# Optimization experiments

Measured on AMD Instinct MI355X. Metric: run time of the kernel, lower is better.

Reference implementation:

```python
import jax, jax.numpy as jnp
import numpy as np

D_IN, D_HID, N_TOK = 2048, 8192, 8192

def _ternary(key, shape):
    # ternary {-1, 0, 1} weights stored as float32
    return jax.random.randint(key, shape, -1, 2).astype(jnp.float32)

def setup_inputs() -> dict:
    key = jax.random.key(0)
    kx, k1, k2, kh, k3 = jax.random.split(key, 5)
    return {
        "x": jax.random.normal(kx, (N_TOK, D_IN), dtype=jnp.float32),
        "W1": _ternary(k1, (D_HID, D_IN)),   # gate proj
        "W2": _ternary(k2, (D_HID, D_IN)),   # value proj
        "Wh": _ternary(kh, (D_HID, D_HID)),  # hidden layer (depth-1 == 1)
        "W3": _ternary(k3, (D_IN, D_HID)),   # output proj
        # per-layer dequant scales (scalar), ~1/sqrt(fan_in)
        "s1": jnp.float32(1.0 / np.sqrt(D_IN)),
        "s2": jnp.float32(1.0 / np.sqrt(D_IN)),
        "sh": jnp.float32(1.0 / np.sqrt(D_HID)),
        "s3": jnp.float32(1.0 / np.sqrt(D_HID)),
    }

def _tlin(x, W, s):
    # ternary packed linear: dequantized matmul, no bias
    return jnp.einsum('td,hd->th', x, W) * s

def reference(x, W1, W2, Wh, W3, s1, s2, sh, s3):
    h = jax.nn.silu(_tlin(x, W1, s1)) * _tlin(x, W2, s2)   # SwiGLU entry
    h = jax.nn.gelu(_tlin(h, Wh, sh), approximate=False)    # hidden block (depth-1)
    return _tlin(h, W3, s3)                                 # [N_TOK, D_IN]
```

## Files before the change

### kernel.cpp

```cpp
#include <hip/hip_runtime.h>
#include <hip/hip_bf16.h>
#include <stdint.h>

typedef __bf16 bf16;
typedef __bf16 bf16x8 __attribute__((ext_vector_type(8)));
typedef float f32x4 __attribute__((ext_vector_type(4)));

typedef uint32_t __attribute__((address_space(1))) * gptr_as1;
typedef uint32_t __attribute__((address_space(3))) * lptr_as3;

__device__ __forceinline__ void async16(const void* g, void* l) {
    __builtin_amdgcn_global_load_lds((gptr_as1)(uintptr_t)g,
                                     (lptr_as3)(uintptr_t)l,
                                     16, 0, 0);
}

__device__ __forceinline__ void bar() {
    asm volatile("" ::: "memory");
    __builtin_amdgcn_s_barrier();
    asm volatile("" ::: "memory");
}

__global__ void cvt_f32_bf16_kernel(const float* __restrict__ src,
                                    bf16* __restrict__ dst, int n8) {
    int i = blockIdx.x * blockDim.x + threadIdx.x;
    if (i >= n8) return;
    const float4* s = reinterpret_cast<const float4*>(src);
    float4 a = s[2 * (size_t)i], b = s[2 * (size_t)i + 1];
    bf16x8 v;
    v[0] = (bf16)a.x; v[1] = (bf16)a.y; v[2] = (bf16)a.z; v[3] = (bf16)a.w;
    v[4] = (bf16)b.x; v[5] = (bf16)b.y; v[6] = (bf16)b.z; v[7] = (bf16)b.w;
    *reinterpret_cast<bf16x8*>(dst + (size_t)i * 8) = v;
}

__global__ void cvt_ilv_kernel(const float* __restrict__ src,
                               bf16* __restrict__ dst, int n8, int sel) {
    int i = blockIdx.x * blockDim.x + threadIdx.x;
    if (i >= n8) return;
    const int row = i >> 8;
    const int c = i & 255;
    const int drow = ((row >> 4) << 5) + (sel << 4) + (row & 15);
    const float4* s = reinterpret_cast<const float4*>(src);
    float4 a = s[2 * (size_t)i], b = s[2 * (size_t)i + 1];
    bf16x8 v;
    v[0] = (bf16)a.x; v[1] = (bf16)a.y; v[2] = (bf16)a.z; v[3] = (bf16)a.w;
    v[4] = (bf16)b.x; v[5] = (bf16)b.y; v[6] = (bf16)b.z; v[7] = (bf16)b.w;
    *reinterpret_cast<bf16x8*>(dst + ((size_t)drow * 256 + c) * 8) = v;
}

template <int EPI, int K>
__global__ __launch_bounds__(512, 1)
void gemm8p(const bf16* __restrict__ A, const bf16* __restrict__ B,
            void* __restrict__ Cout, const float* __restrict__ s1p,
            const float* __restrict__ s2p, int N, int ldh) {
    __shared__ __align__(16) char sm[131072];

    const int tid = threadIdx.x;
    const int w = tid >> 6, l = tid & 63;
    const int wr = w >> 2, wc = w & 3;

    const int gx = gridDim.x;
    const int nwg = gx * (int)gridDim.y;
    const int orig = blockIdx.y * gx + blockIdx.x;
    const int wg = (orig & 7) * (nwg >> 3) + (orig >> 3);
    const int bm = wg / gx, bn = wg % gx;

    constexpr int NT = K / 64;

    f32x4 acc[8][4] = {};

    char* const bufA0 = sm;
    char* const bufB0 = sm + 32768;
    char* const bufA1 = sm + 65536;
    char* const bufB1 = sm + 98304;
    const int arow = bm * 256, brow = bn * 256;

    const int srow_in = l >> 3;
    const int scolb = ((l & 7) ^ srow_in) << 4;
    auto STAGE = [&](char* ldsT, const bf16* g, int grow0, int kt, int r0) {
        const int rr = r0 + w * 8 + srow_in;
        const char* gp = (const char*)(g + (size_t)(grow0 + rr) * K + kt * 64) + scolb;
        async16(gp, ldsT + r0 * 128 + w * 1024);
    };

    const int rlane = l & 15;
    const int chi = (l >> 4) << 4;
    const int sw = (rlane & 7) << 4;
    const int ksd = (rlane & 4) ? -64 : 64;
    const int offA = (wr * 128 + rlane) * 128 + (chi ^ sw);
    const int offB = (wc * 64 + rlane) * 128 + (chi ^ sw);
    const char* const pA0  = bufA0 + offA;  const char* const pA0k = pA0 + ksd;
    const char* const pB0  = bufB0 + offB;  const char* const pB0k = pB0 + ksd;
    const char* const pA1  = bufA1 + offA;  const char* const pA1k = pA1 + ksd;
    const char* const pB1  = bufB1 + offB;  const char* const pB1k = pB1 + ksd;

    STAGE(bufA0, A, arow, 0, 0);   STAGE(bufA0, A, arow, 0, 128);
    STAGE(bufB0, B, brow, 0, 0);   STAGE(bufB0, B, brow, 0, 64);
    STAGE(bufB0, B, brow, 0, 128); STAGE(bufB0, B, brow, 0, 192);
    STAGE(bufA0, A, arow, 0, 64);  STAGE(bufA0, A, arow, 0, 192);
    STAGE(bufA1, A, arow, 1, 0);   STAGE(bufA1, A, arow, 1, 128);
    STAGE(bufB1, B, brow, 1, 0);   STAGE(bufB1, B, brow, 1, 64);
    STAGE(bufB1, B, brow, 1, 128); STAGE(bufB1, B, brow, 1, 192);
    asm volatile("s_waitcnt vmcnt(6)" ::: "memory");
    bar();

    auto body = [&](int kt, char* cA, char* cB, char* nA,
                    const char* pa, const char* pak,
                    const char* pb, const char* pbk) {
        bf16x8 ae[4], ao[4], bv[4];
#pragma unroll
        for (int i = 0; i < 4; ++i)
            ae[i] = *reinterpret_cast<const bf16x8*>(pa + i * 2048);
#pragma unroll
        for (int j = 0; j < 4; ++j)
            bv[j] = *reinterpret_cast<const bf16x8*>(pb + j * 2048);
        if (kt + 1 < NT) { STAGE(nA, A, arow, kt + 1, 64); STAGE(nA, A, arow, kt + 1, 192); }
        bar();
        asm volatile("s_waitcnt lgkmcnt(0)" ::: "memory");
        __builtin_amdgcn_sched_barrier(0);
        __builtin_amdgcn_s_setprio(1);
#pragma unroll
        for (int i = 0; i < 4; ++i)
#pragma unroll
            for (int j = 0; j < 4; ++j)
                acc[i][j] = __builtin_amdgcn_mfma_f32_16x16x32_bf16(ae[i], bv[j], acc[i][j], 0, 0, 0);
        __builtin_amdgcn_s_setprio(0);
        bar();
#pragma unroll
        for (int i = 0; i < 4; ++i)
            ao[i] = *reinterpret_cast<const bf16x8*>(pa + 8192 + i * 2048);
        bar();
        asm volatile("s_waitcnt lgkmcnt(0)" ::: "memory");
        __builtin_amdgcn_sched_barrier(0);
        __builtin_amdgcn_s_setprio(1);
#pragma unroll
        for (int i = 0; i < 4; ++i)
#pragma unroll
            for (int j = 0; j < 4; ++j)
                acc[4 + i][j] = __builtin_amdgcn_mfma_f32_16x16x32_bf16(ao[i], bv[j], acc[4 + i][j], 0, 0, 0);
        __builtin_amdgcn_s_setprio(0);
        bar();
#pragma unroll
        for (int i = 0; i < 4; ++i)
            ae[i] = *reinterpret_cast<const bf16x8*>(pak + i * 2048);
#pragma unroll
        for (int j = 0; j < 4; ++j)
            bv[j] = *reinterpret_cast<const bf16x8*>(pbk + j * 2048);
        if (kt + 2 < NT) { STAGE(cB, B, brow, kt + 2, 0); STAGE(cB, B, brow, kt + 2, 64); }
        bar();
        asm volatile("s_waitcnt lgkmcnt(0)" ::: "memory");
        __builtin_amdgcn_sched_barrier(0);
        __builtin_amdgcn_s_setprio(1);
#pragma unroll
        for (int i = 0; i < 4; ++i)
#pragma unroll
            for (int j = 0; j < 4; ++j)
                acc[i][j] = __builtin_amdgcn_mfma_f32_16x16x32_bf16(ae[i], bv[j], acc[i][j], 0, 0, 0);
        __builtin_amdgcn_s_setprio(0);
        bar();
#pragma unroll
        for (int i = 0; i < 4; ++i)
            ao[i] = *reinterpret_cast<const bf16x8*>(pak + 8192 + i * 2048);
        if (kt + 2 < NT) {
            STAGE(cB, B, brow, kt + 2, 128); STAGE(cB, B, brow, kt + 2, 192);
            STAGE(cA, A, arow, kt + 2, 0);   STAGE(cA, A, arow, kt + 2, 128);
        }
        bar();
        asm volatile("s_waitcnt lgkmcnt(0)" ::: "memory");
        __builtin_amdgcn_sched_barrier(0);
        __builtin_amdgcn_s_setprio(1);
#pragma unroll
        for (int i = 0; i < 4; ++i)
#pragma unroll
            for (int j = 0; j < 4; ++j)
                acc[4 + i][j] = __builtin_amdgcn_mfma_f32_16x16x32_bf16(ao[i], bv[j], acc[4 + i][j], 0, 0, 0);
        __builtin_amdgcn_s_setprio(0);
        if (kt == NT - 2) { asm volatile("s_waitcnt vmcnt(0)" ::: "memory"); }
        else              { asm volatile("s_waitcnt vmcnt(6)" ::: "memory"); }
        bar();
    };

#pragma unroll 1
    for (int kt = 0; kt < NT; kt += 2) {
        body(kt,     bufA0, bufB0, bufA1, pA0, pA0k, pB0, pB0k);
        body(kt + 1, bufA1, bufB1, bufA0, pA1, pA1k, pB1, pB1k);
    }

    const float s1 = s1p[0];
    const int r0 = bm * 256 + wr * 128 + ((l >> 4) << 2);
    if constexpr (EPI == 2) {
        const float s2 = s2p[0];
        const int hcb = (bn * 8 + wc * 2) * 16 + rlane;
#pragma unroll
        for (int i = 0; i < 8; ++i)
#pragma unroll
            for (int jp = 0; jp < 2; ++jp)
#pragma unroll
                for (int q = 0; q < 4; ++q) {
                    float g = acc[i][2 * jp][q] * s1;
                    float v = acc[i][2 * jp + 1][q] * s2;
                    float sig = 1.0f / (1.0f + __expf(-g));
                    ((bf16*)Cout)[(size_t)(r0 + i * 16 + q) * ldh + hcb + jp * 16] =
                        (bf16)(g * sig * v);
                }
    } else {
        const int c0 = bn * 256 + wc * 64 + rlane;
#pragma unroll
        for (int i = 0; i < 8; ++i)
#pragma unroll
            for (int j = 0; j < 4; ++j)
#pragma unroll
                for (int q = 0; q < 4; ++q) {
                    float v = acc[i][j][q] * s1;
                    size_t idx = (size_t)(r0 + i * 16 + q) * N + (c0 + j * 16);
                    if constexpr (EPI == 0) {
                        float g = 0.5f * v * (1.0f + erff(v * 0.70710678118654752f));
                        ((bf16*)Cout)[idx] = (bf16)g;
                    } else {
                        ((float*)Cout)[idx] = v;
                    }
                }
    }
}

extern "C" void kernel_launch(void* const* d_in, const int* in_sizes, int n_in,
                              void* d_out, int out_size, void* d_ws, size_t ws_size,
                              hipStream_t stream) {
    constexpr int NTOK = 8192, DIN = 2048, DHID = 8192;

    const float* x  = (const float*)d_in[0];
    const float* W1 = (const float*)d_in[1];
    const float* W2 = (const float*)d_in[2];
    const float* Wh = (const float*)d_in[3];
    const float* W3 = (const float*)d_in[4];
    const float* s1 = (const float*)d_in[5];
    const float* s2 = (const float*)d_in[6];
    const float* sh = (const float*)d_in[7];
    const float* s3 = (const float*)d_in[8];
    float* out = (float*)d_out;

    char* ws = (char*)d_ws;
    size_t off = 0;
    bf16* xb   = (bf16*)(ws + off); off += (size_t)NTOK * DIN * 2;
    bf16* w12b = (bf16*)(ws + off); off += (size_t)2 * DHID * DIN * 2;
    bf16* w3b  = (bf16*)(ws + off); off += (size_t)DIN * DHID * 2;
    bf16* whb  = (bf16*)(ws + off); off += (size_t)DHID * DHID * 2;
    bf16* h1   = (bf16*)(ws + off); off += (size_t)NTOK * DHID * 2;
    bf16* h2   = (bf16*)(ws + off); off += (size_t)NTOK * DHID * 2;
    if (ws_size < off) return;

    auto cvt = [&](const float* s, bf16* d, size_t n) {
        int n8 = (int)(n / 8);
        cvt_f32_bf16_kernel<<<(n8 + 255) / 256, 256, 0, stream>>>(s, d, n8);
    };
    cvt(x,  xb,  (size_t)NTOK * DIN);
    cvt(Wh, whb, (size_t)DHID * DHID);
    cvt(W3, w3b, (size_t)DIN * DHID);
    {
        int n8 = (int)((size_t)DHID * DIN / 8);
        cvt_ilv_kernel<<<(n8 + 255) / 256, 256, 0, stream>>>(W1, w12b, n8, 0);
        cvt_ilv_kernel<<<(n8 + 255) / 256, 256, 0, stream>>>(W2, w12b, n8, 1);
    }

    gemm8p<2, DIN><<<dim3(2 * DHID / 256, NTOK / 256), 512, 0, stream>>>(
        xb, w12b, h1, s1, s2, 2 * DHID, DHID);
    gemm8p<0, DHID><<<dim3(DHID / 256, NTOK / 256), 512, 0, stream>>>(
        h1, whb, h2, sh, sh, DHID, DHID);
    gemm8p<1, DHID><<<dim3(DIN / 256, NTOK / 256), 512, 0, stream>>>(
        h2, w3b, out, s3, s3, DIN, DIN);
}
```

Baseline: 1.713 ms.

## Use 256x128-tile two-waves-per-SIMD GEMM kernel for hidden layer

Adds a new GEMM kernel with 256-thread blocks, 256x128 output tiles, K-step 32, a double-buffered 48KB LDS and launch bounds allowing two blocks per CU. The hidden-layer GEMM now uses it instead of the 512-thread 256x256 kernel. The aim is to hide latency through occupancy across co-resident blocks rather than deep intra-block pipelining. The trade-off is less operand reuse per tile and more barriers per unit of K.

```diff
diff --git a/kernel.cpp b/kernel.cpp
--- a/kernel.cpp
+++ b/kernel.cpp
@@ -49,6 +49,127 @@
 }
 
 template <int EPI, int K>
+__global__ __launch_bounds__(256, 2)
+void gemm2t(const bf16* __restrict__ A, const bf16* __restrict__ B,
+            void* __restrict__ Cout, const float* __restrict__ s1p,
+            const float* __restrict__ s2p, int N, int ldh) {
+    __shared__ __align__(16) char sm[49152];
+
+    const int tid = threadIdx.x;
+    const int w = tid >> 6, l = tid & 63;
+    const int wr = w >> 1, wc = w & 1;
+
+    const int gx = gridDim.x;
+    const int nwg = gx * (int)gridDim.y;
+    const int orig = blockIdx.y * gx + blockIdx.x;
+    const int wg = (orig & 7) * (nwg >> 3) + (orig >> 3);
+    const int bm = wg / gx, bn = wg % gx;
+
+    constexpr int NT = K / 32;
+
+    f32x4 acc[8][4] = {};
+
+    const int arow = bm * 256, brow = bn * 128;
+
+    const int sr = l >> 2;
+    const int sg = ((l & 3) ^ ((l >> 3) & 3)) << 4;
+    const char* qa0 = (const char*)(A + (size_t)(arow +   0 + w * 16 + sr) * K) + sg;
+    const char* qa1 = (const char*)(A + (size_t)(arow +  64 + w * 16 + sr) * K) + sg;
+    const char* qa2 = (const char*)(A + (size_t)(arow + 128 + w * 16 + sr) * K) + sg;
+    const char* qa3 = (const char*)(A + (size_t)(arow + 192 + w * 16 + sr) * K) + sg;
+    const char* qb0 = (const char*)(B + (size_t)(brow +   0 + w * 16 + sr) * K) + sg;
+    const char* qb1 = (const char*)(B + (size_t)(brow +  64 + w * 16 + sr) * K) + sg;
+    const int ldw = w * 1024;
+
+    auto STAGE_TILE = [&](int p) {
+        char* ba = sm + p * 24576;
+        char* bb = ba + 16384;
+        async16(qa0, ba +     0 + ldw); async16(qa1, ba +  4096 + ldw);
+        async16(qa2, ba +  8192 + ldw); async16(qa3, ba + 12288 + ldw);
+        async16(qb0, bb +     0 + ldw); async16(qb1, bb +  4096 + ldw);
+    };
+    auto ADV = [&]() {
+        qa0 += 64; qa1 += 64; qa2 += 64; qa3 += 64; qb0 += 64; qb1 += 64;
+    };
+
+    const int rlane = l & 15;
+    const int chi = (l >> 4) << 4;
+
+    STAGE_TILE(0);
+    ADV();
+    asm volatile("s_waitcnt vmcnt(0)" ::: "memory");
+    bar();
+
+#pragma unroll 1
+    for (int kt = 0; kt < NT; ++kt) {
+        if (kt + 1 < NT) { STAGE_TILE((kt + 1) & 1); ADV(); }
+        const char* ba = sm + (kt & 1) * 24576;
+        const char* bb = ba + 16384;
+
+        bf16x8 av[8], bv[4];
+#pragma unroll
+        for (int i = 0; i < 8; ++i) {
+            const int row = wr * 128 + i * 16 + rlane;
+            av[i] = *reinterpret_cast<const bf16x8*>(
+                ba + row * 64 + (chi ^ (((row >> 1) & 3) << 4)));
+        }
+#pragma unroll
+        for (int j = 0; j < 4; ++j) {
+            const int row = wc * 64 + j * 16 + rlane;
+            bv[j] = *reinterpret_cast<const bf16x8*>(
+                bb + row * 64 + (chi ^ (((row >> 1) & 3) << 4)));
+        }
+        asm volatile("s_waitcnt lgkmcnt(0)" ::: "memory");
+        __builtin_amdgcn_sched_barrier(0);
+        __builtin_amdgcn_s_setprio(1);
+#pragma unroll
+        for (int i = 0; i < 8; ++i)
+#pragma unroll
+            for (int j = 0; j < 4; ++j)
+                acc[i][j] = __builtin_amdgcn_mfma_f32_16x16x32_bf16(av[i], bv[j], acc[i][j], 0, 0, 0);
+        __builtin_amdgcn_s_setprio(0);
+        asm volatile("s_waitcnt vmcnt(0)" ::: "memory");
+        bar();
+    }
+
+    const float s1 = s1p[0];
+    const int r0 = bm * 256 + wr * 128 + ((l >> 4) << 2);
+    if constexpr (EPI == 2) {
+        const float s2 = s2p[0];
+        const int hcb = (bn * 4 + wc * 2) * 16 + rlane;
+#pragma unroll
+        for (int i = 0; i < 8; ++i)
+#pragma unroll
+            for (int jp = 0; jp < 2; ++jp)
+#pragma unroll
+                for (int q = 0; q < 4; ++q) {
+                    float g = acc[i][2 * jp][q] * s1;
+                    float v = acc[i][2 * jp + 1][q] * s2;
+                    float sig = 1.0f / (1.0f + __expf(-g));
+                    ((bf16*)Cout)[(size_t)(r0 + i * 16 + q) * ldh + hcb + jp * 16] =
+                        (bf16)(g * sig * v);
+                }
+    } else {
+        const int c0 = bn * 128 + wc * 64 + rlane;
+#pragma unroll
+        for (int i = 0; i < 8; ++i)
+#pragma unroll
+            for (int j = 0; j < 4; ++j)
+#pragma unroll
+                for (int q = 0; q < 4; ++q) {
+                    float v = acc[i][j][q] * s1;
+                    size_t idx = (size_t)(r0 + i * 16 + q) * N + (c0 + j * 16);
+                    if constexpr (EPI == 0) {
+                        float g = 0.5f * v * (1.0f + erff(v * 0.70710678118654752f));
+                        ((bf16*)Cout)[idx] = (bf16)g;
+                    } else {
+                        ((float*)Cout)[idx] = v;
+                    }
+                }
+    }
+}
+
+template <int EPI, int K>
 __global__ __launch_bounds__(512, 1)
 void gemm8p(const bf16* __restrict__ A, const bf16* __restrict__ B,
             void* __restrict__ Cout, const float* __restrict__ s1p,
@@ -264,7 +385,7 @@
 
     gemm8p<2, DIN><<<dim3(2 * DHID / 256, NTOK / 256), 512, 0, stream>>>(
         xb, w12b, h1, s1, s2, 2 * DHID, DHID);
-    gemm8p<0, DHID><<<dim3(DHID / 256, NTOK / 256), 512, 0, stream>>>(
+    gemm2t<0, DHID><<<dim3(DHID / 128, NTOK / 256), 256, 0, stream>>>(
         h1, whb, h2, sh, sh, DHID, DHID);
     gemm8p<1, DHID><<<dim3(DIN / 256, NTOK / 256), 512, 0, stream>>>(
         h2, w3b, out, s3, s3, DIN, DIN);
```

Measured after the change: 1.890 ms. +10.3%, slower.
